# Optimization experiments

Measured on AMD Instinct MI355X. Metric: run time of the kernel, lower is better.

Reference implementation:

```python
import jax, jax.numpy as jnp
import numpy as np
import math

D_MODEL = 2048
N_HEADS = 16
D_HEAD = D_MODEL // N_HEADS
SCALE = 1.0 / math.sqrt(D_HEAD)


def setup_inputs() -> dict:
    key = jax.random.key(0)
    kx, kq, kk, kv, ko = jax.random.split(key, 5)
    x = jax.random.normal(kx, (2, 2048, D_MODEL), dtype=jnp.float32)
    W_q = jax.random.normal(kq, (D_MODEL, D_MODEL), dtype=jnp.float32)
    W_k = jax.random.normal(kk, (D_MODEL, D_MODEL), dtype=jnp.float32)
    W_v = jax.random.normal(kv, (D_MODEL, D_MODEL), dtype=jnp.float32) * math.sqrt(2.0 / D_MODEL)
    W_o = jax.random.normal(ko, (D_MODEL, D_MODEL), dtype=jnp.float32) * math.sqrt(2.0 / D_MODEL)
    return {"x": x, "W_q": W_q, "W_k": W_k, "W_v": W_v, "W_o": W_o}


def reference(x, W_q, W_k, W_v, W_o) -> jnp.ndarray:
    B, S, D = x.shape
    q = (x @ W_q).reshape(B, S, N_HEADS, D_HEAD)  # [b, q, h, dh]
    k = (x @ W_k).reshape(B, S, N_HEADS, D_HEAD)  # [b, k, h, dh]
    v = x @ W_v                                    # [b, k, d_model] (NOT split into heads)
    scores = jnp.einsum('bqhd,bkhd->bhqk', q, k)   # [b, h, q, k]
    # Faithful quirk: additive -1e9 causal mask applied BEFORE the scale.
    mask = jnp.triu(jnp.full((S, S), -1e9, dtype=scores.dtype), k=1)
    scores = (scores + mask) * SCALE
    probs = jax.nn.softmax(scores, axis=-1)
    # Faithful quirk: sums over heads h AND keys k against full-width v.
    out = jnp.einsum('bhqk,bkd->bqd', probs, v)    # [b, q, d_model]
    return out @ W_o
```

## Files before the change

kernel.cpp:

```cpp
#include <hip/hip_runtime.h>

typedef unsigned short u16;
typedef __attribute__((ext_vector_type(8))) short bf16x8;
typedef __attribute__((ext_vector_type(4))) float f32x4;

#define DEV __device__ __forceinline__

DEV u16 f2bf(float f) {
  union { float f; unsigned u; } v; v.f = f;
  unsigned r = v.u + 0x7fffu + ((v.u >> 16) & 1u);
  return (u16)(r >> 16);
}
DEV float bf2f(u16 h) {
  union { unsigned u; float f; } v; v.u = ((unsigned)h) << 16;
  return v.f;
}
DEV f32x4 mfma16(bf16x8 a, bf16x8 b, f32x4 c) {
  return __builtin_amdgcn_mfma_f32_16x16x32_bf16(a, b, c, 0, 0, 0);
}
DEV void cp16(const u16* g, u16* l) {
  __builtin_amdgcn_global_load_lds((__attribute__((address_space(1))) void*)g,
                                   (__attribute__((address_space(3))) void*)l, 16, 0, 0);
}

__global__ __launch_bounds__(256) void split_pair(const float4* __restrict__ x,
                                                  u16* __restrict__ hi, u16* __restrict__ lo) {
  const size_t i = (size_t)blockIdx.x * 256 + threadIdx.x;
  const float4 v = x[i];
  ushort4 h, l;
  h.x = f2bf(v.x); l.x = f2bf(v.x - bf2f(h.x));
  h.y = f2bf(v.y); l.y = f2bf(v.y - bf2f(h.y));
  h.z = f2bf(v.z); l.z = f2bf(v.z - bf2f(h.z));
  h.w = f2bf(v.w); l.w = f2bf(v.w - bf2f(h.w));
  *(ushort4*)&hi[i * 4] = h;
  *(ushort4*)&lo[i * 4] = l;
}

template<bool LO>
__global__ __launch_bounds__(256) void transpose_split(const float* __restrict__ W,
                                                       u16* __restrict__ Th, u16* __restrict__ Tl) {
  __shared__ float t[64][65];
  const int r0 = blockIdx.y * 64, c0 = blockIdx.x * 64;
  const int rr = threadIdx.x >> 4, c4 = (threadIdx.x & 15) * 4;
#pragma unroll
  for (int p = 0; p < 4; ++p) {
    const float4 v = *(const float4*)&W[(size_t)(r0 + p * 16 + rr) * 2048 + c0 + c4];
    t[p * 16 + rr][c4 + 0] = v.x; t[p * 16 + rr][c4 + 1] = v.y;
    t[p * 16 + rr][c4 + 2] = v.z; t[p * 16 + rr][c4 + 3] = v.w;
  }
  __syncthreads();
#pragma unroll
  for (int p = 0; p < 4; ++p) {
    const int cc = p * 16 + rr;
    const float v0 = t[c4 + 0][cc], v1 = t[c4 + 1][cc], v2 = t[c4 + 2][cc], v3 = t[c4 + 3][cc];
    ushort4 h;
    h.x = f2bf(v0); h.y = f2bf(v1); h.z = f2bf(v2); h.w = f2bf(v3);
    *(ushort4*)&Th[(size_t)(c0 + cc) * 2048 + r0 + c4] = h;
    if constexpr (LO) {
      ushort4 l;
      l.x = f2bf(v0 - bf2f(h.x)); l.y = f2bf(v1 - bf2f(h.y));
      l.z = f2bf(v2 - bf2f(h.z)); l.w = f2bf(v3 - bf2f(h.w));
      *(ushort4*)&Tl[(size_t)(c0 + cc) * 2048 + r0 + c4] = l;
    }
  }
}

template<bool SPLIT3, int OUTMODE, bool KLIM>
__global__ __launch_bounds__(256, 2) void gemm_bt(
    const u16* __restrict__ Aph, const u16* __restrict__ Apl,
    const u16* __restrict__ Bph, const u16* __restrict__ Bpl,
    void* __restrict__ C0, void* __restrict__ C1,
    const int M, const int N, const int K, const int bShift) {
  extern __shared__ u16 lds[];
  constexpr int T_AL = 4096;
  constexpr int T_BH = SPLIT3 ? 8192 : 4096;
  constexpr int T_BL = 12288;
  const int tid = threadIdx.x;
  const int wave = tid >> 6, lane = tid & 63;
  const int li = lane & 15, l4 = lane >> 4;
  const int m0 = blockIdx.y * 128, n0 = blockIdx.x * 128;
  const int wr = (wave >> 1) * 64, wc = (wave & 1) * 64;
  const u16* Bh = Bph; const u16* Bl = Bpl;
  if (bShift) { const size_t s = (size_t)(m0 >> 11) * (size_t)bShift; Bh += s; if (SPLIT3) Bl += s; }

  const f32x4 fz = {0.f, 0.f, 0.f, 0.f};
  f32x4 acc[4][4];
#pragma unroll
  for (int m = 0; m < 4; ++m)
#pragma unroll
    for (int n = 0; n < 4; ++n) acc[m][n] = fz;

  const size_t aoff = (size_t)(m0 + (tid >> 2)) * K + (tid & 3) * 8;
  const size_t boff = (size_t)(n0 + (tid >> 2)) * K + (tid & 3) * 8;
  const size_t rstep = (size_t)64 * K;
  const int s0 = tid * 8, s1 = 2048 + tid * 8;
  const int abase = (wr + li) * 32 + l4 * 8;
  const int bbase = (wc + li) * 32 + l4 * 8;
  const int kEnd = KLIM ? ((m0 & 2047) + 128 < K ? (m0 & 2047) + 128 : K) : K;

#pragma unroll 1
  for (int k0 = 0; k0 < kEnd; k0 += 32) {
    cp16(Aph + aoff + k0,         &lds[s0]);
    cp16(Aph + aoff + rstep + k0, &lds[s1]);
    cp16(Bh + boff + k0,          &lds[T_BH + s0]);
    cp16(Bh + boff + rstep + k0,  &lds[T_BH + s1]);
    if constexpr (SPLIT3) {
      cp16(Apl + aoff + k0,         &lds[T_AL + s0]);
      cp16(Apl + aoff + rstep + k0, &lds[T_AL + s1]);
      cp16(Bl + boff + k0,          &lds[T_BL + s0]);
      cp16(Bl + boff + rstep + k0,  &lds[T_BL + s1]);
    }
    __syncthreads();
    bf16x8 af[4], bf_[4];
#pragma unroll
    for (int m = 0; m < 4; ++m) af[m] = *(const bf16x8*)&lds[abase + m * 512];
#pragma unroll
    for (int n = 0; n < 4; ++n) bf_[n] = *(const bf16x8*)&lds[T_BH + bbase + n * 512];
    if constexpr (SPLIT3) {
      bf16x8 alf[4], blf[4];
#pragma unroll
      for (int m = 0; m < 4; ++m) alf[m] = *(const bf16x8*)&lds[T_AL + abase + m * 512];
#pragma unroll
      for (int n = 0; n < 4; ++n) blf[n] = *(const bf16x8*)&lds[T_BL + bbase + n * 512];
#pragma unroll
      for (int m = 0; m < 4; ++m)
#pragma unroll
        for (int n = 0; n < 4; ++n) {
          acc[m][n] = mfma16(af[m], bf_[n], acc[m][n]);
          acc[m][n] = mfma16(af[m], blf[n], acc[m][n]);
          acc[m][n] = mfma16(alf[m], bf_[n], acc[m][n]);
        }
    } else {
#pragma unroll
      for (int m = 0; m < 4; ++m)
#pragma unroll
        for (int n = 0; n < 4; ++n)
          acc[m][n] = mfma16(af[m], bf_[n], acc[m][n]);
    }
    __syncthreads();
  }

#pragma unroll
  for (int m = 0; m < 4; ++m) {
#pragma unroll
    for (int n = 0; n < 4; ++n) {
      const int rg0 = m0 + wr + m * 16 + l4 * 4;
      const int cg  = n0 + wc + n * 16 + li;
      if constexpr (OUTMODE == 0) {
        u16* Ch = (u16*)C0; u16* Cl = (u16*)C1;
#pragma unroll
        for (int r = 0; r < 4; ++r) {
          const float v = acc[m][n][r];
          const u16 h = f2bf(v);
          Ch[(size_t)(rg0 + r) * N + cg] = h;
          Cl[(size_t)(rg0 + r) * N + cg] = f2bf(v - bf2f(h));
        }
      } else if constexpr (OUTMODE == 1) {
        u16* Cs = (u16*)C0;
#pragma unroll
        for (int r = 0; r < 4; ++r) Cs[(size_t)(rg0 + r) * N + cg] = f2bf(acc[m][n][r]);
      } else if constexpr (OUTMODE == 2) {
        u16* Vt = (u16*)C0;
        ushort4 pk;
        pk.x = f2bf(acc[m][n][0]); pk.y = f2bf(acc[m][n][1]);
        pk.z = f2bf(acc[m][n][2]); pk.w = f2bf(acc[m][n][3]);
        *(ushort4*)&Vt[(size_t)(rg0 >> 11) * 4194304 + (size_t)cg * 2048 + (rg0 & 2047)] = pk;
      } else {
        float* Cf = (float*)C0;
#pragma unroll
        for (int r = 0; r < 4; ++r) Cf[(size_t)(rg0 + r) * N + cg] = acc[m][n][r];
      }
    }
  }
}

#define C2EXP 0.1275174381027786f

__global__ __launch_bounds__(256) void attn_lse(
    const u16* __restrict__ Qh, const u16* __restrict__ Ql,
    const u16* __restrict__ Kh, const u16* __restrict__ Kl,
    float* __restrict__ LSE) {
  __shared__ __align__(16) u16 kb[16384];
  const int tid = threadIdx.x, wave = tid >> 6, lane = tid & 63;
  const int li = lane & 15, l4 = lane >> 4;
  const int qt = 15 - (int)blockIdx.x, h = blockIdx.y, b = blockIdx.z;
  const int q0w = qt * 128 + wave * 32;

  bf16x8 qfh[2][4], qfl[2][4];
#pragma unroll
  for (int mf = 0; mf < 2; ++mf) {
    const size_t qo = ((size_t)(b * 2048 + q0w + mf * 16 + li)) * 2048 + h * 128 + l4 * 8;
#pragma unroll
    for (int ks = 0; ks < 4; ++ks) {
      qfh[mf][ks] = *(const bf16x8*)&Qh[qo + ks * 32];
      qfl[mf][ks] = *(const bf16x8*)&Ql[qo + ks * 32];
    }
  }
  float m[2][4], l[2][4];
#pragma unroll
  for (int mf = 0; mf < 2; ++mf)
#pragma unroll
    for (int r = 0; r < 4; ++r) { m[mf][r] = -3.0e38f; l[mf][r] = 0.f; }

  const int nsub = qt * 2 + 2;
  const size_t kgbase = ((size_t)b * 2048) * 2048 + h * 128;
#pragma unroll 1
  for (int t = 0; t < nsub; ++t) {
    __syncthreads();
#pragma unroll
    for (int i = 0; i < 4; ++i) {
      const int e = (tid + i * 256) * 8;
      const int dck = e >> 11, s = (e >> 5) & 63, dl = e & 31;
      const size_t g = kgbase + (size_t)(t * 64 + s) * 2048 + dck * 32 + dl;
      cp16(Kh + g, kb + e);
      cp16(Kl + g, kb + 8192 + e);
    }
    __syncthreads();
#pragma unroll
    for (int mf = 0; mf < 2; ++mf) {
#pragma unroll
      for (int sn = 0; sn < 4; ++sn) {
        f32x4 a = {0.f, 0.f, 0.f, 0.f};
        const int fo = (sn * 16 + li) * 32 + l4 * 8;
#pragma unroll
        for (int ks = 0; ks < 4; ++ks) {
          const bf16x8 kfh = *(const bf16x8*)&kb[ks * 2048 + fo];
          const bf16x8 kfl = *(const bf16x8*)&kb[8192 + ks * 2048 + fo];
          a = mfma16(qfh[mf][ks], kfh, a);
          a = mfma16(qfh[mf][ks], kfl, a);
          a = mfma16(qfl[mf][ks], kfh, a);
        }
        const int kg = t * 64 + sn * 16 + li;
#pragma unroll
        for (int r = 0; r < 4; ++r) {
          if (kg <= q0w + mf * 16 + l4 * 4 + r) {
            const float mn = fmaxf(m[mf][r], a[r]);
            l[mf][r] = l[mf][r] * exp2f((m[mf][r] - mn) * C2EXP) + exp2f((a[r] - mn) * C2EXP);
            m[mf][r] = mn;
          }
        }
      }
    }
  }
#pragma unroll
  for (int off = 1; off <= 8; off <<= 1) {
#pragma unroll
    for (int mf = 0; mf < 2; ++mf)
#pragma unroll
      for (int r = 0; r < 4; ++r) {
        const float om = __shfl_xor(m[mf][r], off, 64);
        const float ol = __shfl_xor(l[mf][r], off, 64);
        const float mn = fmaxf(m[mf][r], om);
        l[mf][r] = l[mf][r] * exp2f((m[mf][r] - mn) * C2EXP) + ol * exp2f((om - mn) * C2EXP);
        m[mf][r] = mn;
      }
  }
  if (li == 0) {
#pragma unroll
    for (int mf = 0; mf < 2; ++mf)
#pragma unroll
      for (int r = 0; r < 4; ++r)
        LSE[(size_t)(b * 16 + h) * 2048 + q0w + mf * 16 + l4 * 4 + r] =
            m[mf][r] * C2EXP + log2f(l[mf][r]);
  }
}

__global__ __launch_bounds__(256) void attn_psum(
    const u16* __restrict__ Qh, const u16* __restrict__ Ql,
    const u16* __restrict__ Kh, const u16* __restrict__ Kl,
    const float* __restrict__ LSE, u16* __restrict__ Psum) {
  const int kt = blockIdx.x, qt = blockIdx.y, b = blockIdx.z;
  const int q0 = qt * 128, k0 = kt * 128;
  const int tid = threadIdx.x;

  if (kt > qt) {
    const size_t o = ((size_t)(b * 2048 + q0 + (tid >> 1))) * 2048 + k0 + (tid & 1) * 64;
    const uint4 z = {0u, 0u, 0u, 0u};
#pragma unroll
    for (int j = 0; j < 8; ++j) *(uint4*)&Psum[o + j * 8] = z;
    return;
  }

  extern __shared__ u16 kb2[];
  const int wave = tid >> 6, lane = tid & 63;
  const int li = lane & 15, l4 = lane >> 4;
  const int q0w = q0 + wave * 32;

  const f32x4 fz = {0.f, 0.f, 0.f, 0.f};
  f32x4 ps[2][8];
#pragma unroll
  for (int mf = 0; mf < 2; ++mf)
#pragma unroll
    for (int sn = 0; sn < 8; ++sn) ps[mf][sn] = fz;

  const size_t kgbase = ((size_t)(b * 2048 + k0)) * 2048;
  const size_t qbase0 = ((size_t)(b * 2048 + q0w + li)) * 2048 + l4 * 8;
  const size_t qbase1 = qbase0 + (size_t)16 * 2048;
  const size_t lbase  = (size_t)(b * 16) * 2048 + q0w + l4 * 4;

#pragma unroll 1
  for (int h = 0; h < 16; ++h) {
    __syncthreads();
#pragma unroll
    for (int i = 0; i < 8; ++i) {
      const int e = (tid + i * 256) * 8;
      const int dck = e >> 12, s = (e >> 5) & 127, dl = e & 31;
      const size_t g = kgbase + (size_t)s * 2048 + h * 128 + dck * 32 + dl;
      cp16(Kh + g, kb2 + e);
      cp16(Kl + g, kb2 + 16384 + e);
    }
    bf16x8 qfh[2][4], qfl[2][4];
    float clse[2][4];
#pragma unroll
    for (int ks = 0; ks < 4; ++ks) {
      qfh[0][ks] = *(const bf16x8*)&Qh[qbase0 + (size_t)h * 128 + ks * 32];
      qfl[0][ks] = *(const bf16x8*)&Ql[qbase0 + (size_t)h * 128 + ks * 32];
      qfh[1][ks] = *(const bf16x8*)&Qh[qbase1 + (size_t)h * 128 + ks * 32];
      qfl[1][ks] = *(const bf16x8*)&Ql[qbase1 + (size_t)h * 128 + ks * 32];
    }
#pragma unroll
    for (int mf = 0; mf < 2; ++mf)
#pragma unroll
      for (int r = 0; r < 4; ++r)
        clse[mf][r] = LSE[lbase + (size_t)h * 2048 + mf * 16 + r];
    __syncthreads();

#pragma unroll
    for (int mf = 0; mf < 2; ++mf) {
      const int snlim = (kt == qt) ? (wave * 2 + mf + 1) : 8;
#pragma unroll
      for (int sn = 0; sn < 8; ++sn) {
        if (sn >= snlim) continue;
        f32x4 a = {0.f, 0.f, 0.f, 0.f};
        const int fo = (sn * 16 + li) * 32 + l4 * 8;
#pragma unroll
        for (int ks = 0; ks < 4; ++ks) {
          const bf16x8 kfh = *(const bf16x8*)&kb2[ks * 4096 + fo];
          const bf16x8 kfl = *(const bf16x8*)&kb2[16384 + ks * 4096 + fo];
          a = mfma16(qfh[mf][ks], kfh, a);
          a = mfma16(qfh[mf][ks], kfl, a);
          a = mfma16(qfl[mf][ks], kfh, a);
        }
        const int kg = k0 + sn * 16 + li;
#pragma unroll
        for (int r = 0; r < 4; ++r) {
          if (kg <= q0w + mf * 16 + l4 * 4 + r)
            ps[mf][sn][r] += exp2f(a[r] * C2EXP - clse[mf][r]);
        }
      }
    }
  }

#pragma unroll
  for (int mf = 0; mf < 2; ++mf)
#pragma unroll
    for (int sn = 0; sn < 8; ++sn) {
      const size_t o0 = ((size_t)(b * 2048 + q0w + mf * 16 + l4 * 4)) * 2048 + k0 + sn * 16 + li;
#pragma unroll
      for (int r = 0; r < 4; ++r) Psum[o0 + (size_t)r * 2048] = f2bf(ps[mf][sn][r]);
    }
}

extern "C" void kernel_launch(void* const* d_in, const int* in_sizes, int n_in,
                              void* d_out, int out_size, void* d_ws, size_t ws_size,
                              hipStream_t stream) {
  (void)in_sizes; (void)n_in; (void)out_size; (void)ws_size;
  const float* x  = (const float*)d_in[0];
  const float* Wq = (const float*)d_in[1];
  const float* Wk = (const float*)d_in[2];
  const float* Wv = (const float*)d_in[3];
  const float* Wo = (const float*)d_in[4];
  u16* ws = (u16*)d_ws;
  const size_t E8 = 8388608, E4 = 4194304;
  u16* xh = ws;
  u16* xl = ws + E8;
  u16* Qh = ws + 2 * E8;
  u16* Ql = ws + 3 * E8;
  u16* Kh = ws + 4 * E8;
  u16* Kl = ws + 5 * E8;
  u16* Vt = ws + 6 * E8;
  u16* WTh = ws + 7 * E8;
  u16* WTl = ws + 7 * E8 + E4;
  u16* WTb = ws + 7 * E8 + 2 * E4;
  float* LSEf = (float*)WTl;
  u16* Psum = xl;
  u16* out1 = xh;

  split_pair<<<8192, 256, 0, stream>>>((const float4*)x, xh, xl);

  dim3 tg(32, 32);
  dim3 gg(16, 32);

  transpose_split<true ><<<tg, 256, 0, stream>>>(Wq, WTh, WTl);
  gemm_bt<true, 0, false><<<gg, 256, 32768, stream>>>(xh, xl, WTh, WTl, Qh, Ql, 4096, 2048, 2048, 0);

  transpose_split<true ><<<tg, 256, 0, stream>>>(Wk, WTh, WTl);
  gemm_bt<true, 0, false><<<gg, 256, 32768, stream>>>(xh, xl, WTh, WTl, Kh, Kl, 4096, 2048, 2048, 0);

  transpose_split<false><<<tg, 256, 0, stream>>>(Wv, WTb, nullptr);
  gemm_bt<false, 2, false><<<gg, 256, 16384, stream>>>(xh, nullptr, WTb, nullptr, Vt, nullptr, 4096, 2048, 2048, 0);

  attn_lse <<<dim3(16, 16, 2), 256, 0, stream>>>(Qh, Ql, Kh, Kl, LSEf);
  attn_psum<<<dim3(16, 16, 2), 256, 65536, stream>>>(Qh, Ql, Kh, Kl, LSEf, Psum);

  gemm_bt<false, 1, true><<<gg, 256, 16384, stream>>>(Psum, nullptr, Vt, nullptr, out1, nullptr, 4096, 2048, 2048, 4194304);

  transpose_split<false><<<tg, 256, 0, stream>>>(Wo, WTb, nullptr);
  gemm_bt<false, 3, false><<<gg, 256, 16384, stream>>>(out1, nullptr, WTb, nullptr, d_out, nullptr, 4096, 2048, 2048, 0);
}
```

Before: 655.0 us.

## Split LSE pass over key chunks, swizzle LDS, and use fast exp2

The log-sum-exp kernel now splits each query tile's key range into up to four chunks, each handled by its own block, and writes partial max and sum values. A new merge kernel combines them, which balances the causal workload and raises grid parallelism. Both attention kernels also XOR-swizzle the K tile layout in LDS to avoid bank conflicts, interleave the two query fragments so each K fragment load feeds six MFMAs, and replace exp2f/log2f with the hardware intrinsics. The cost is an extra launch, extra partial buffers in the workspace, and slightly lower exp precision.

```diff
diff --git a/kernel.cpp b/kernel.cpp
--- a/kernel.cpp
+++ b/kernel.cpp
@@ -5,6 +5,8 @@
 typedef __attribute__((ext_vector_type(4))) float f32x4;
 
 #define DEV __device__ __forceinline__
+#define EXP2(x) __builtin_amdgcn_exp2f(x)
+#define LOG2(x) __builtin_amdgcn_logf(x)
 
 DEV u16 f2bf(float f) {
   union { float f; unsigned u; } v; v.f = f;
@@ -176,15 +178,26 @@
 
 #define C2EXP 0.1275174381027786f
 
-__global__ __launch_bounds__(256) void attn_lse(
+__global__ __launch_bounds__(256) void attn_lse_part(
     const u16* __restrict__ Qh, const u16* __restrict__ Ql,
     const u16* __restrict__ Kh, const u16* __restrict__ Kl,
-    float* __restrict__ LSE) {
+    float* __restrict__ Mp, float* __restrict__ Lp) {
+  const int j = blockIdx.x, qt = 15 - (int)blockIdx.y, hb = blockIdx.z;
+  const int b = hb >> 4, h = hb & 15;
+  const int tid = threadIdx.x;
+  const int nch = (qt >> 2) + 1;
+  if (j >= nch) {
+    if (tid < 128) {
+      const size_t o = ((size_t)hb * 4 + j) * 2048 + qt * 128 + tid;
+      Mp[o] = -3.0e38f; Lp[o] = 0.f;
+    }
+    return;
+  }
   __shared__ __align__(16) u16 kb[16384];
-  const int tid = threadIdx.x, wave = tid >> 6, lane = tid & 63;
+  const int wave = tid >> 6, lane = tid & 63;
   const int li = lane & 15, l4 = lane >> 4;
-  const int qt = 15 - (int)blockIdx.x, h = blockIdx.y, b = blockIdx.z;
   const int q0w = qt * 128 + wave * 32;
+  const int rs = ((li << 6) | (l4 << 4)) ^ (((li >> 1) & 7) << 4);
 
   bf16x8 qfh[2][4], qfl[2][4];
 #pragma unroll
@@ -202,42 +215,50 @@
 #pragma unroll
     for (int r = 0; r < 4; ++r) { m[mf][r] = -3.0e38f; l[mf][r] = 0.f; }
 
-  const int nsub = qt * 2 + 2;
+  const int kst = j * 8;
+  const int ken = min(j * 8 + 8, qt * 2 + 2);
   const size_t kgbase = ((size_t)b * 2048) * 2048 + h * 128;
+  const f32x4 fz = {0.f, 0.f, 0.f, 0.f};
+
 #pragma unroll 1
-  for (int t = 0; t < nsub; ++t) {
+  for (int t = kst; t < ken; ++t) {
     __syncthreads();
 #pragma unroll
     for (int i = 0; i < 4; ++i) {
-      const int e = (tid + i * 256) * 8;
-      const int dck = e >> 11, s = (e >> 5) & 63, dl = e & 31;
+      const int o = (tid + i * 256) * 16;
+      const int op = o ^ (((o >> 7) & 7) << 4);
+      const int dck = op >> 12, s = (op >> 6) & 63, dl = (op >> 1) & 31;
       const size_t g = kgbase + (size_t)(t * 64 + s) * 2048 + dck * 32 + dl;
-      cp16(Kh + g, kb + e);
-      cp16(Kl + g, kb + 8192 + e);
-    }
-    __syncthreads();
-#pragma unroll
-    for (int mf = 0; mf < 2; ++mf) {
-#pragma unroll
-      for (int sn = 0; sn < 4; ++sn) {
-        f32x4 a = {0.f, 0.f, 0.f, 0.f};
-        const int fo = (sn * 16 + li) * 32 + l4 * 8;
-#pragma unroll
-        for (int ks = 0; ks < 4; ++ks) {
-          const bf16x8 kfh = *(const bf16x8*)&kb[ks * 2048 + fo];
-          const bf16x8 kfl = *(const bf16x8*)&kb[8192 + ks * 2048 + fo];
-          a = mfma16(qfh[mf][ks], kfh, a);
-          a = mfma16(qfh[mf][ks], kfl, a);
-          a = mfma16(qfl[mf][ks], kfh, a);
-        }
-        const int kg = t * 64 + sn * 16 + li;
-#pragma unroll
-        for (int r = 0; r < 4; ++r) {
-          if (kg <= q0w + mf * 16 + l4 * 4 + r) {
-            const float mn = fmaxf(m[mf][r], a[r]);
-            l[mf][r] = l[mf][r] * exp2f((m[mf][r] - mn) * C2EXP) + exp2f((a[r] - mn) * C2EXP);
-            m[mf][r] = mn;
-          }
+      cp16(Kh + g, kb + (o >> 1));
+      cp16(Kl + g, kb + 8192 + (o >> 1));
+    }
+    __syncthreads();
+#pragma unroll
+    for (int sn = 0; sn < 4; ++sn) {
+      f32x4 a0 = fz, a1 = fz;
+#pragma unroll
+      for (int ks = 0; ks < 4; ++ks) {
+        const bf16x8 kh = *(const bf16x8*)((const char*)kb + ks * 4096 + (sn << 10) + rs);
+        const bf16x8 kl = *(const bf16x8*)((const char*)kb + 16384 + ks * 4096 + (sn << 10) + rs);
+        a0 = mfma16(qfh[0][ks], kh, a0);
+        a0 = mfma16(qfh[0][ks], kl, a0);
+        a0 = mfma16(qfl[0][ks], kh, a0);
+        a1 = mfma16(qfh[1][ks], kh, a1);
+        a1 = mfma16(qfh[1][ks], kl, a1);
+        a1 = mfma16(qfl[1][ks], kh, a1);
+      }
+      const int kg = t * 64 + sn * 16 + li;
+#pragma unroll
+      for (int r = 0; r < 4; ++r) {
+        if (kg <= q0w + l4 * 4 + r) {
+          const float mn = fmaxf(m[0][r], a0[r]);
+          l[0][r] = l[0][r] * EXP2((m[0][r] - mn) * C2EXP) + EXP2((a0[r] - mn) * C2EXP);
+          m[0][r] = mn;
+        }
+        if (kg <= q0w + 16 + l4 * 4 + r) {
+          const float mn = fmaxf(m[1][r], a1[r]);
+          l[1][r] = l[1][r] * EXP2((m[1][r] - mn) * C2EXP) + EXP2((a1[r] - mn) * C2EXP);
+          m[1][r] = mn;
         }
       }
     }
@@ -251,7 +272,7 @@
         const float om = __shfl_xor(m[mf][r], off, 64);
         const float ol = __shfl_xor(l[mf][r], off, 64);
         const float mn = fmaxf(m[mf][r], om);
-        l[mf][r] = l[mf][r] * exp2f((m[mf][r] - mn) * C2EXP) + ol * exp2f((om - mn) * C2EXP);
+        l[mf][r] = l[mf][r] * EXP2((m[mf][r] - mn) * C2EXP) + ol * EXP2((om - mn) * C2EXP);
         m[mf][r] = mn;
       }
   }
@@ -259,10 +280,29 @@
 #pragma unroll
     for (int mf = 0; mf < 2; ++mf)
 #pragma unroll
-      for (int r = 0; r < 4; ++r)
-        LSE[(size_t)(b * 16 + h) * 2048 + q0w + mf * 16 + l4 * 4 + r] =
-            m[mf][r] * C2EXP + log2f(l[mf][r]);
-  }
+      for (int r = 0; r < 4; ++r) {
+        const size_t o = ((size_t)hb * 4 + j) * 2048 + q0w + mf * 16 + l4 * 4 + r;
+        Mp[o] = m[mf][r];
+        Lp[o] = l[mf][r];
+      }
+  }
+}
+
+__global__ __launch_bounds__(256) void attn_lse_merge(
+    const float* __restrict__ Mp, const float* __restrict__ Lp, float* __restrict__ LSE) {
+  const int id = blockIdx.x * 256 + threadIdx.x;
+  const int q = id & 2047, hb = id >> 11;
+  const size_t base = (size_t)hb * 4 * 2048 + q;
+  float m = Mp[base], l = Lp[base];
+#pragma unroll
+  for (int jj = 1; jj < 4; ++jj) {
+    const float om = Mp[base + jj * 2048];
+    const float ol = Lp[base + jj * 2048];
+    const float mn = fmaxf(m, om);
+    l = l * EXP2((m - mn) * C2EXP) + ol * EXP2((om - mn) * C2EXP);
+    m = mn;
+  }
+  LSE[(size_t)hb * 2048 + q] = m * C2EXP + LOG2(l);
 }
 
 __global__ __launch_bounds__(256) void attn_psum(
@@ -285,6 +325,8 @@
   const int wave = tid >> 6, lane = tid & 63;
   const int li = lane & 15, l4 = lane >> 4;
   const int q0w = q0 + wave * 32;
+  const int rs = ((li << 6) | (l4 << 4)) ^ (((li >> 1) & 7) << 4);
+  const int snmax = (kt == qt) ? (wave * 2 + 2) : 8;
 
   const f32x4 fz = {0.f, 0.f, 0.f, 0.f};
   f32x4 ps[2][8];
@@ -303,20 +345,21 @@
     __syncthreads();
 #pragma unroll
     for (int i = 0; i < 8; ++i) {
-      const int e = (tid + i * 256) * 8;
-      const int dck = e >> 12, s = (e >> 5) & 127, dl = e & 31;
+      const int o = (tid + i * 256) * 16;
+      const int op = o ^ (((o >> 7) & 7) << 4);
+      const int dck = op >> 13, s = (op >> 6) & 127, dl = (op >> 1) & 31;
       const size_t g = kgbase + (size_t)s * 2048 + h * 128 + dck * 32 + dl;
-      cp16(Kh + g, kb2 + e);
-      cp16(Kl + g, kb2 + 16384 + e);
-    }
-    bf16x8 qfh[2][4], qfl[2][4];
+      cp16(Kh + g, kb2 + (o >> 1));
+      cp16(Kl + g, kb2 + 16384 + (o >> 1));
+    }
+    bf16x8 qfh0[4], qfl0[4], qfh1[4], qfl1[4];
     float clse[2][4];
 #pragma unroll
     for (int ks = 0; ks < 4; ++ks) {
-      qfh[0][ks] = *(const bf16x8*)&Qh[qbase0 + (size_t)h * 128 + ks * 32];
-      qfl[0][ks] = *(const bf16x8*)&Ql[qbase0 + (size_t)h * 128 + ks * 32];
-      qfh[1][ks] = *(const bf16x8*)&Qh[qbase1 + (size_t)h * 128 + ks * 32];
-      qfl[1][ks] = *(const bf16x8*)&Ql[qbase1 + (size_t)h * 128 + ks * 32];
+      qfh0[ks] = *(const bf16x8*)&Qh[qbase0 + (size_t)h * 128 + ks * 32];
+      qfl0[ks] = *(const bf16x8*)&Ql[qbase0 + (size_t)h * 128 + ks * 32];
+      qfh1[ks] = *(const bf16x8*)&Qh[qbase1 + (size_t)h * 128 + ks * 32];
+      qfl1[ks] = *(const bf16x8*)&Ql[qbase1 + (size_t)h * 128 + ks * 32];
     }
 #pragma unroll
     for (int mf = 0; mf < 2; ++mf)
@@ -326,26 +369,25 @@
     __syncthreads();
 
 #pragma unroll
-    for (int mf = 0; mf < 2; ++mf) {
-      const int snlim = (kt == qt) ? (wave * 2 + mf + 1) : 8;
-#pragma unroll
-      for (int sn = 0; sn < 8; ++sn) {
-        if (sn >= snlim) continue;
-        f32x4 a = {0.f, 0.f, 0.f, 0.f};
-        const int fo = (sn * 16 + li) * 32 + l4 * 8;
+    for (int sn = 0; sn < 8; ++sn) {
+      if (sn < snmax) {
+        f32x4 a0 = fz, a1 = fz;
 #pragma unroll
         for (int ks = 0; ks < 4; ++ks) {
-          const bf16x8 kfh = *(const bf16x8*)&kb2[ks * 4096 + fo];
-          const bf16x8 kfl = *(const bf16x8*)&kb2[16384 + ks * 4096 + fo];
-          a = mfma16(qfh[mf][ks], kfh, a);
-          a = mfma16(qfh[mf][ks], kfl, a);
-          a = mfma16(qfl[mf][ks], kfh, a);
+          const bf16x8 kh = *(const bf16x8*)((const char*)kb2 + ks * 8192 + (sn << 10) + rs);
+          const bf16x8 kl = *(const bf16x8*)((const char*)kb2 + 32768 + ks * 8192 + (sn << 10) + rs);
+          a0 = mfma16(qfh0[ks], kh, a0);
+          a0 = mfma16(qfh0[ks], kl, a0);
+          a0 = mfma16(qfl0[ks], kh, a0);
+          a1 = mfma16(qfh1[ks], kh, a1);
+          a1 = mfma16(qfh1[ks], kl, a1);
+          a1 = mfma16(qfl1[ks], kh, a1);
         }
         const int kg = k0 + sn * 16 + li;
 #pragma unroll
         for (int r = 0; r < 4; ++r) {
-          if (kg <= q0w + mf * 16 + l4 * 4 + r)
-            ps[mf][sn][r] += exp2f(a[r] * C2EXP - clse[mf][r]);
+          if (kg <= q0w + l4 * 4 + r)      ps[0][sn][r] += EXP2(a0[r] * C2EXP - clse[0][r]);
+          if (kg <= q0w + 16 + l4 * 4 + r) ps[1][sn][r] += EXP2(a1[r] * C2EXP - clse[1][r]);
         }
       }
     }
@@ -383,6 +425,8 @@
   u16* WTl = ws + 7 * E8 + E4;
   u16* WTb = ws + 7 * E8 + 2 * E4;
   float* LSEf = (float*)WTl;
+  float* Mp   = LSEf + 65536;
+  float* Lp   = Mp + 262144;
   u16* Psum = xl;
   u16* out1 = xh;
 
@@ -400,7 +444,8 @@
   transpose_split<false><<<tg, 256, 0, stream>>>(Wv, WTb, nullptr);
   gemm_bt<false, 2, false><<<gg, 256, 16384, stream>>>(xh, nullptr, WTb, nullptr, Vt, nullptr, 4096, 2048, 2048, 0);
 
-  attn_lse <<<dim3(16, 16, 2), 256, 0, stream>>>(Qh, Ql, Kh, Kl, LSEf);
+  attn_lse_part<<<dim3(4, 16, 32), 256, 0, stream>>>(Qh, Ql, Kh, Kl, Mp, Lp);
+  attn_lse_merge<<<256, 256, 0, stream>>>(Mp, Lp, LSEf);
   attn_psum<<<dim3(16, 16, 2), 256, 65536, stream>>>(Qh, Ql, Kh, Kl, LSEf, Psum);
 
   gemm_bt<false, 1, true><<<gg, 256, 16384, stream>>>(Psum, nullptr, Vt, nullptr, out1, nullptr, 4096, 2048, 2048, 4194304);
```

Result: faster. 602.1 us (-8.1%).
